# Optimization experiments

Measured on AMD Instinct MI355X. Metric: run time of the kernel, lower is better.

Reference implementation:

```python
import jax, jax.numpy as jnp
import numpy as np

F_DIM = 64
USER_SIZES = [11577, 11, 11, 11, 11, 21, 7]
URL_SIZES = [4733, 21, 7, 11, 11]
USER_OFF = np.concatenate([[0], np.cumsum(USER_SIZES)[:-1]]).astype(np.int64)
URL_OFF = np.concatenate([[0], np.cumsum(URL_SIZES)[:-1]]).astype(np.int64)
EPS = 1e-6


def feature_embed(table, offsets, feats):
    # feats: [..., F] int ids per feature column; sum of per-column embeddings -> [..., F_DIM]
    return jnp.take(table, feats + offsets, axis=0).sum(axis=-2)


def cosine(a, b):
    # cosine similarity along last axis, torch-style eps clamping of each norm
    dot = jnp.sum(a * b, axis=-1)
    na = jnp.maximum(jnp.sqrt(jnp.sum(a * a, axis=-1)), EPS)
    nb = jnp.maximum(jnp.sqrt(jnp.sum(b * b, axis=-1)), EPS)
    return dot / (na * nb)


def graph_attention(f_embed, weight_list, center_embed):
    # f_embed: [..., K, D], weight_list: [..., K], center_embed: [..., D]
    cw = cosine(f_embed, jnp.expand_dims(center_embed, -2))      # [..., K]
    cw = jax.nn.softmax(cw, axis=-1)
    new = jax.nn.relu(f_embed * weight_list[..., None]) * cw[..., None]
    return new.sum(axis=-2)                                      # [..., D]


def linear(x, W, b):
    return x @ W.T + b


def setup_inputs() -> dict:
    key = jax.random.key(0)
    ks = jax.random.split(key, 24)
    N, K = 8192, 8
    ri = lambda k, shp, hi: jax.random.randint(k, shp, 0, hi, dtype=jnp.int64)
    rf = lambda k, shp: jax.random.uniform(k, shp, dtype=jnp.float32)
    rn = lambda k, shp, s: jax.random.normal(k, shp, dtype=jnp.float32) * s
    inp = {
        'url_idxs': ri(ks[0], (N,), 4733),
        'user_f_list': ri(ks[1], (N, 7), 7),
        'url_f_list': ri(ks[2], (N, 5), 7),
        'user_1_user_f_list': ri(ks[3], (N, K, 7), 7),
        'user_1_user_weight': rf(ks[4], (N, K)),
        'user_1_url_f_list': ri(ks[5], (N, K, 5), 7),
        'user_1_url_weight': rf(ks[6], (N, K)),
        'user_2_user_f_list': ri(ks[7], (N, K, K, 7), 7),
        'user_2_user_weight': rf(ks[8], (N, K, K)),
        'user_2_url_f_list': ri(ks[9], (N, K, K, 5), 7),
        'user_2_url_weight': rf(ks[10], (N, K, K)),
        'url_2_user_f_list': ri(ks[11], (N, K, K, 7), 7),
        'url_2_user_weight': rf(ks[12], (N, K, K)),
        'url_2_url_f_list': ri(ks[13], (N, K, K, 5), 7),
        'url_2_url_weight': rf(ks[14], (N, K, K)),
        'user_table': rn(ks[15], (int(sum(USER_SIZES)), F_DIM), 0.1),
        'url_table': rn(ks[16], (int(sum(URL_SIZES)), F_DIM), 0.1),
        'W2': rn(ks[17], (F_DIM, 2 * F_DIM), 0.05), 'b2': jnp.zeros((F_DIM,), jnp.float32),
        'W1': rn(ks[18], (F_DIM, 2 * F_DIM), 0.05), 'b1': jnp.zeros((F_DIM,), jnp.float32),
        'Wo': rn(ks[19], (2, 2 * F_DIM), 0.05), 'bo': jnp.zeros((2,), jnp.float32),
    }
    return inp


def reference(url_idxs, user_f_list, url_f_list,
              user_1_user_f_list, user_1_user_weight,
              user_1_url_f_list, user_1_url_weight,
              user_2_user_f_list, user_2_user_weight,
              user_2_url_f_list, user_2_url_weight,
              url_2_user_f_list, url_2_user_weight,
              url_2_url_f_list, url_2_url_weight,
              user_table, url_table, W2, b2, W1, b1, Wo, bo):
    user_off = jnp.asarray(USER_OFF)
    url_off = jnp.asarray(URL_OFF)

    # --- url branch (hop2 -> hop1) ---
    ori_user_1_url = feature_embed(url_table, url_off, user_1_url_f_list)        # [N,K,D]
    ori_url_2_user = feature_embed(user_table, user_off, url_2_user_f_list)      # [N,K,K,D]
    url_2_user_new = graph_attention(ori_url_2_user, url_2_user_weight, ori_user_1_url)
    ori_url_2_url = feature_embed(url_table, url_off, url_2_url_f_list)
    url_2_url_new = graph_attention(ori_url_2_url, url_2_url_weight, ori_user_1_url)
    user_1_url = (url_2_user_new + url_2_url_new) / 2
    user_1_url = jax.nn.relu(linear(jnp.concatenate([ori_user_1_url, user_1_url], axis=2), W2, b2))

    # --- user branch (hop2 -> hop1) ---
    ori_user_1_user = feature_embed(user_table, user_off, user_1_user_f_list)
    ori_user_2_user = feature_embed(user_table, user_off, user_2_user_f_list)
    user_2_user_new = graph_attention(ori_user_2_user, user_2_user_weight, ori_user_1_user)
    ori_user_2_url = feature_embed(url_table, url_off, user_2_url_f_list)
    user_2_url_new = graph_attention(ori_user_2_url, user_2_url_weight, ori_user_1_user)
    user_1_user = (user_2_user_new + user_2_url_new) / 2
    user_1_user = jax.nn.relu(linear(jnp.concatenate([ori_user_1_user, user_1_user], axis=2), W2, b2))

    # --- hop1 -> center ---
    ori_user = feature_embed(user_table, user_off, user_f_list)                  # [N,D]
    u1_url_new = graph_attention(user_1_url, user_1_url_weight, ori_user)
    u1_user_new = graph_attention(user_1_user, user_1_user_weight, ori_user)
    user_embed = (u1_url_new + u1_user_new) / 2
    user_embed = jax.nn.relu(linear(jnp.concatenate([ori_user, user_embed], axis=1), W1, b1))

    url_embed = feature_embed(url_table, url_off, url_f_list)                    # [N,D]
    out = linear(jnp.concatenate([user_embed, url_embed], axis=1), Wo, bo)       # [N,2]
    return jax.nn.softmax(out, axis=1)
```

## Files before the change

kernel.cpp:

```cpp
#include <hip/hip_runtime.h>

#define TPB 256
#define SPB 4
#define NSAMP 8192

#if __has_builtin(__builtin_amdgcn_rcpf)
#define RCPF(x) __builtin_amdgcn_rcpf(x)
#else
#define RCPF(x) (1.0f/(x))
#endif
#if __has_builtin(__builtin_amdgcn_rsqf)
#define RSQF(x) __builtin_amdgcn_rsqf(x)
#else
#define RSQF(x) rsqrtf(x)
#endif

#define O_CENT   0
#define O_CRN    1024
#define O_ORI    1040
#define O_ORN    1104
#define O_URLEMB 1108
#define O_JOB    1172
#define O_H1     2196
#define O_PIDX   3220
#define O_W      3428
#define O_GA1    3684
#define O_PART   3812
#define O_W1H    4068
#define O_CIDX   4084
#define DYN_SZ   4096

__device__ __forceinline__ float sx(float v, int m) { return __shfl_xor(v, m, 64); }

template <int CTRL>
__device__ __forceinline__ float dpp_add(float v) {
  return v + __int_as_float(__builtin_amdgcn_update_dpp(
      0, __float_as_int(v), CTRL, 0xf, 0xf, true));
}
__device__ __forceinline__ float red16(float v) {
  v = dpp_add<0xB1>(v);
  v = dpp_add<0x4E>(v);
  v = dpp_add<0x141>(v);
  v = dpp_add<0x140>(v);
  return v;
}

__global__ __launch_bounds__(TPB, 3)
void gcn_fused(const int* __restrict__ g_user_f, const int* __restrict__ g_url_f,
               const int* __restrict__ g_u1u_f, const float* __restrict__ g_u1u_w,
               const int* __restrict__ g_u1l_f, const float* __restrict__ g_u1l_w,
               const int* __restrict__ g_u2u_f, const float* __restrict__ g_u2u_w,
               const int* __restrict__ g_u2l_f, const float* __restrict__ g_u2l_w,
               const int* __restrict__ g_l2u_f, const float* __restrict__ g_l2u_w,
               const int* __restrict__ g_l2l_f, const float* __restrict__ g_l2l_w,
               const float* __restrict__ g_utab, const float* __restrict__ g_ltab,
               const float* __restrict__ g_W2, const float* __restrict__ g_b2,
               const float* __restrict__ g_W1, const float* __restrict__ g_b1,
               const float* __restrict__ g_Wo, const float* __restrict__ g_bo,
               float* __restrict__ g_out)
{
  __shared__ __align__(16) float s_lut[5376];
  __shared__ __align__(16) float s_dyn[DYN_SZ];

  const int tid  = threadIdx.x;
  const int wv   = tid >> 6;
  const int lane = tid & 63;
  const int g    = (tid >> 4) & 3;
  const int l    = tid & 15;

  float* s_ulut = s_lut;
  float* s_llut = s_lut + 49*64;
  int*   s_pidx = (int*)&s_dyn[O_PIDX];
  int*   s_cidx = (int*)&s_dyn[O_CIDX];
  float* s_h1   = &s_dyn[O_H1];

  float w2r[32];
  for (int half = 0; half < 2; ++half) {
    for (int i = tid; i < 4096; i += TPB) {
      const int r = i >> 7, j = i & 127;
      s_lut[r*132 + j] = g_W2[(half*32 + r)*128 + j];
    }
    __syncthreads();
    if ((lane >> 5) == half) {
      const int lr = lane & 31;
      #pragma unroll
      for (int jj = 0; jj < 32; ++jj)
        w2r[jj] = s_lut[lr*132 + wv*32 + jj];
    }
    __syncthreads();
  }

  {
    constexpr int uoff[7] = {0,11577,11588,11599,11610,11621,11642};
    #pragma unroll
    for (int c = 0; c < 7; ++c)
      for (int i = tid; i < 448; i += TPB)
        s_ulut[c*448 + i] = g_utab[(uoff[c] + (i >> 6))*64 + (i & 63)];
    constexpr int loff[5] = {0,4733,4754,4761,4772};
    #pragma unroll
    for (int c = 0; c < 5; ++c)
      for (int i = tid; i < 448; i += TPB)
        s_llut[c*448 + i] = g_ltab[(loff[c] + (i >> 6))*64 + (i & 63)];
  }

  const float b2v = g_b2[lane];

  const int  jb      = wv;
  const bool F7      = (jb == 0 || jb == 2);
  const int  F3      = F7 ? 7 : 5;
  const float* lut3  = F7 ? s_ulut : s_llut;
  const int  nibbase = (jb == 0) ? 768 : (jb == 1) ? 1216 : (jb == 2) ? 0 : 448;
  const int  b3      = jb >> 1;

  #pragma unroll 1
  for (int s = 0; s < SPB; ++s) {
    const int n = blockIdx.x * SPB + s;
    __syncthreads();

    if (tid < 192) {
      const int w = tid;
      const int* ptr; int rel;
      if (w < 56)       { ptr = g_u2u_f + n*448; rel = w; }
      else if (w < 96)  { ptr = g_u2l_f + n*320; rel = w - 56; }
      else if (w < 152) { ptr = g_l2u_f + n*448; rel = w - 96; }
      else              { ptr = g_l2l_f + n*320; rel = w - 152; }
      const int4 a = *(const int4*)(ptr + rel*8);
      const int4 b = *(const int4*)(ptr + rel*8 + 4);
      s_pidx[w] = (a.x&7) | ((a.y&7)<<4) | ((a.z&7)<<8) | ((a.w&7)<<12)
                | ((b.x&7)<<16) | ((b.y&7)<<20) | ((b.z&7)<<24) | ((b.w&7)<<28);
    } else if (tid < 204) {
      const int w = tid - 192;
      const int* ptr; int rel;
      if (w < 7) { ptr = g_u1u_f + n*56; rel = w; } else { ptr = g_u1l_f + n*40; rel = w - 7; }
      const int4 a = *(const int4*)(ptr + rel*8);
      const int4 b = *(const int4*)(ptr + rel*8 + 4);
      s_pidx[192 + w] = (a.x&7) | ((a.y&7)<<4) | ((a.z&7)<<8) | ((a.w&7)<<12)
                      | ((b.x&7)<<16) | ((b.y&7)<<20) | ((b.z&7)<<24) | ((b.w&7)<<28);
    } else if (tid < 216) {
      const int t = tid - 204;
      s_cidx[t] = (t < 7) ? g_user_f[n*7 + t] : g_url_f[n*5 + (t - 7)];
    } else if (tid < 232) {
      const int t = tid - 216;
      s_dyn[O_W1H + t] = (t < 8) ? g_u1u_w[n*8 + t] : g_u1l_w[n*8 + (t - 8)];
    }
    if (tid < 64) {
      const float* wp = (tid < 16) ? g_l2u_w : (tid < 32) ? g_l2l_w
                       : (tid < 48) ? g_u2u_w : g_u2l_w;
      *(float4*)&s_dyn[O_W + (tid >> 4)*64 + (tid & 15)*4] =
          *(const float4*)&wp[n*64 + (tid & 15)*4];
    }
    *(float4*)&s_dyn[O_JOB + tid*4] = make_float4(0.f, 0.f, 0.f, 0.f);
    #pragma unroll
    for (int r = 0; r < 4; ++r) s_h1[(wv*4 + r)*64 + lane] = b2v;
    __syncthreads();

    {
      const int gg = tid >> 4;
      const bool isUser = gg >= 8;
      const int k = gg & 7;
      const float* lut = isUser ? s_ulut : s_llut;
      const int nb = isUser ? (1536 + k*7) : (1592 + k*5);
      const int wq = nb >> 3;
      unsigned long long u =
          ((unsigned long long)(unsigned)s_pidx[wq + 1] << 32) | (unsigned)s_pidx[wq];
      u >>= ((nb & 7) << 2);
      float4 e = make_float4(0.f,0.f,0.f,0.f);
      if (isUser) {
        #pragma unroll
        for (int c = 0; c < 7; ++c) {
          const int id = (int)(u >> (c*4)) & 7;
          const float4 t = *(const float4*)&lut[((c*7 + id) << 6) + (l << 2)];
          e.x += t.x; e.y += t.y; e.z += t.z; e.w += t.w;
        }
      } else {
        #pragma unroll
        for (int c = 0; c < 5; ++c) {
          const int id = (int)(u >> (c*4)) & 7;
          const float4 t = *(const float4*)&lut[((c*7 + id) << 6) + (l << 2)];
          e.x += t.x; e.y += t.y; e.z += t.z; e.w += t.w;
        }
      }
      float na2 = e.x*e.x + e.y*e.y + e.z*e.z + e.w*e.w;
      na2 = red16(na2);
      const int bsel = isUser ? 1 : 0;
      *(float4*)&s_dyn[O_CENT + bsel*512 + k*64 + l*4] = e;
      if (l == 0) s_dyn[O_CRN + bsel*8 + k] = RSQF(fmaxf(na2, 1e-12f));

      if (gg < 2) {
        const float* lutm = (gg == 0) ? s_ulut : s_llut;
        const int Fm  = (gg == 0) ? 7 : 5;
        const int ibm = (gg == 0) ? 0 : 7;
        float4 em = make_float4(0.f,0.f,0.f,0.f);
        for (int c = 0; c < Fm; ++c) {
          const int id = s_cidx[ibm + c];
          const float4 t = *(const float4*)&lutm[((c*7 + id) << 6) + (l << 2)];
          em.x += t.x; em.y += t.y; em.z += t.z; em.w += t.w;
        }
        if (gg == 0) {
          float nn = em.x*em.x + em.y*em.y + em.z*em.z + em.w*em.w;
          nn = red16(nn);
          *(float4*)&s_dyn[O_ORI + l*4] = em;
          if (l == 0) s_dyn[O_ORN] = RSQF(fmaxf(nn, 1e-12f));
        } else {
          *(float4*)&s_dyn[O_URLEMB + l*4] = em;
        }
      }
    }
    __syncthreads();

    {
      const float* wb = &s_dyn[O_W + jb*64];
      for (int k1 = 0; k1 < 8; ++k1) {
        const float4 c4 = *(const float4*)&s_dyn[O_CENT + b3*512 + k1*64 + l*4];
        const float rnb = s_dyn[O_CRN + b3*8 + k1];
        float4 ek0, ek1; float cs0, cs1;
        #pragma unroll
        for (int p = 0; p < 2; ++p) {
          const int node = k1*8 + p*4 + g;
          const int nb = nibbase + node*F3;
          const int wq = nb >> 3;
          unsigned long long u =
              ((unsigned long long)(unsigned)s_pidx[wq + 1] << 32) | (unsigned)s_pidx[wq];
          u >>= ((nb & 7) << 2);
          float4 e = make_float4(0.f,0.f,0.f,0.f);
          if (F7) {
            #pragma unroll
            for (int c = 0; c < 7; ++c) {
              const int id = (int)(u >> (c*4)) & 7;
              const float4 t = *(const float4*)&lut3[((c*7 + id) << 6) + (l << 2)];
              e.x += t.x; e.y += t.y; e.z += t.z; e.w += t.w;
            }
          } else {
            #pragma unroll
            for (int c = 0; c < 5; ++c) {
              const int id = (int)(u >> (c*4)) & 7;
              const float4 t = *(const float4*)&lut3[((c*7 + id) << 6) + (l << 2)];
              e.x += t.x; e.y += t.y; e.z += t.z; e.w += t.w;
            }
          }
          float dot = e.x*c4.x + e.y*c4.y + e.z*c4.z + e.w*c4.w;
          float na2 = e.x*e.x + e.y*e.y + e.z*e.z + e.w*e.w;
          dot = red16(dot);
          na2 = red16(na2);
          const float cs = dot * RSQF(fmaxf(na2, 1e-12f)) * rnb;
          if (p == 0) { ek0 = e; cs0 = cs; } else { ek1 = e; cs1 = cs; }
        }
        const float ex0 = __expf(cs0), ex1 = __expf(cs1);
        float ss = ex0 + ex1;
        ss += sx(ss, 16); ss += sx(ss, 32);
        const float w0 = wb[k1*8 + g], w1 = wb[k1*8 + 4 + g];
        float ax = fmaxf(ek0.x*w0, 0.f)*ex0 + fmaxf(ek1.x*w1, 0.f)*ex1;
        float ay = fmaxf(ek0.y*w0, 0.f)*ex0 + fmaxf(ek1.y*w1, 0.f)*ex1;
        float az = fmaxf(ek0.z*w0, 0.f)*ex0 + fmaxf(ek1.z*w1, 0.f)*ex1;
        float aw = fmaxf(ek0.w*w0, 0.f)*ex0 + fmaxf(ek1.w*w1, 0.f)*ex1;
        ax += sx(ax,16); ay += sx(ay,16); az += sx(az,16); aw += sx(aw,16);
        ax += sx(ax,32); ay += sx(ay,32); az += sx(az,32); aw += sx(aw,32);
        if (g == 0) {
          const float sc = 0.5f * RCPF(ss);
          float* jp = &s_dyn[O_JOB + b3*512 + k1*64 + l*4];
          atomicAdd(jp + 0, ax*sc);
          atomicAdd(jp + 1, ay*sc);
          atomicAdd(jp + 2, az*sc);
          atomicAdd(jp + 3, aw*sc);
        }
      }
    }
    __syncthreads();

    for (int rr = 0; rr < 16; ++rr) {
      const int branch = rr >> 3, k = rr & 7;
      const float* xp = (wv < 2)
          ? &s_dyn[O_CENT + branch*512 + k*64 + wv*32]
          : &s_dyn[O_JOB  + branch*512 + k*64 + (wv - 2)*32];
      float a = 0.f;
      #pragma unroll
      for (int j4 = 0; j4 < 8; ++j4) {
        const float4 xv = *(const float4*)&xp[j4*4];
        a += xv.x*w2r[j4*4+0] + xv.y*w2r[j4*4+1] + xv.z*w2r[j4*4+2] + xv.w*w2r[j4*4+3];
      }
      atomicAdd(&s_h1[rr*64 + lane], a);
    }
    __syncthreads();
    {
      float4* hp = (float4*)&s_h1[tid*4];
      float4 v = *hp;
      v.x = fmaxf(v.x, 0.f); v.y = fmaxf(v.y, 0.f);
      v.z = fmaxf(v.z, 0.f); v.w = fmaxf(v.w, 0.f);
      *hp = v;
    }
    __syncthreads();

    if (wv < 2) {
      const float4 c4 = *(const float4*)&s_dyn[O_ORI + l*4];
      const float rno = s_dyn[O_ORN];
      const float* h1b = &s_h1[wv*512];
      const int wofs = (wv == 0) ? 8 : 0;
      float4 ek0, ek1; float cs0, cs1;
      #pragma unroll
      for (int p = 0; p < 2; ++p) {
        const int k = p*4 + g;
        const float4 e = *(const float4*)&h1b[k*64 + l*4];
        float dot = e.x*c4.x + e.y*c4.y + e.z*c4.z + e.w*c4.w;
        float na2 = e.x*e.x + e.y*e.y + e.z*e.z + e.w*e.w;
        dot = red16(dot);
        na2 = red16(na2);
        const float cs = dot * RSQF(fmaxf(na2, 1e-12f)) * rno;
        if (p == 0) { ek0 = e; cs0 = cs; } else { ek1 = e; cs1 = cs; }
      }
      const float ex0 = __expf(cs0), ex1 = __expf(cs1);
      float ss = ex0 + ex1;
      ss += sx(ss, 16); ss += sx(ss, 32);
      const float w0 = s_dyn[O_W1H + wofs + g], w1 = s_dyn[O_W1H + wofs + 4 + g];
      float ax = fmaxf(ek0.x*w0, 0.f)*ex0 + fmaxf(ek1.x*w1, 0.f)*ex1;
      float ay = fmaxf(ek0.y*w0, 0.f)*ex0 + fmaxf(ek1.y*w1, 0.f)*ex1;
      float az = fmaxf(ek0.z*w0, 0.f)*ex0 + fmaxf(ek1.z*w1, 0.f)*ex1;
      float aw = fmaxf(ek0.w*w0, 0.f)*ex0 + fmaxf(ek1.w*w1, 0.f)*ex1;
      ax += sx(ax,16); ay += sx(ay,16); az += sx(az,16); aw += sx(aw,16);
      ax += sx(ax,32); ay += sx(ay,32); az += sx(az,32); aw += sx(az,32)*0.f + sx(aw,32);
      if (g == 0) {
        const float sc = 0.5f * RCPF(ss);
        *(float4*)&s_dyn[O_GA1 + wv*64 + l*4] =
            make_float4(ax*sc, ay*sc, az*sc, aw*sc);
      }
    }
    __syncthreads();

    {
      const float* w1p = g_W1 + lane*128 + wv*32;
      float a = 0.f;
      if (wv < 2) {
        const float* xp = &s_dyn[O_ORI + wv*32];
        #pragma unroll
        for (int j4 = 0; j4 < 8; ++j4) {
          const float4 xv = *(const float4*)&xp[j4*4];
          const float4 wq = *(const float4*)&w1p[j4*4];
          a += xv.x*wq.x + xv.y*wq.y + xv.z*wq.z + xv.w*wq.w;
        }
      } else {
        const float* xa = &s_dyn[O_GA1 + (wv - 2)*32];
        const float* xb = &s_dyn[O_GA1 + 64 + (wv - 2)*32];
        #pragma unroll
        for (int j4 = 0; j4 < 8; ++j4) {
          const float4 va = *(const float4*)&xa[j4*4];
          const float4 vb = *(const float4*)&xb[j4*4];
          const float4 wq = *(const float4*)&w1p[j4*4];
          a += (va.x+vb.x)*wq.x + (va.y+vb.y)*wq.y
             + (va.z+vb.z)*wq.z + (va.w+vb.w)*wq.w;
        }
      }
      s_dyn[O_PART + wv*64 + lane] = a;
    }
    __syncthreads();

    if (wv == 0) {
      float ue = g_b1[lane];
      #pragma unroll
      for (int q = 0; q < 4; ++q) ue += s_dyn[O_PART + q*64 + lane];
      ue = fmaxf(ue, 0.f);
      const float ul = s_dyn[O_URLEMB + lane];
      float p0 = ue*g_Wo[lane]     + ul*g_Wo[64 + lane];
      float p1 = ue*g_Wo[128+lane] + ul*g_Wo[192 + lane];
      p0 = red16(p0); p0 += sx(p0, 16); p0 += sx(p0, 32);
      p1 = red16(p1); p1 += sx(p1, 16); p1 += sx(p1, 32);
      if (lane == 0) {
        const float l0 = p0 + g_bo[0], l1 = p1 + g_bo[1];
        const float mx = fmaxf(l0, l1);
        const float q0 = __expf(l0 - mx), q1 = __expf(l1 - mx);
        const float rinv = RCPF(q0 + q1);
        g_out[n*2 + 0] = q0 * rinv;
        g_out[n*2 + 1] = q1 * rinv;
      }
    }
  }
}

extern "C" void kernel_launch(void* const* d_in, const int* in_sizes, int n_in,
                              void* d_out, int out_size, void* d_ws, size_t ws_size,
                              hipStream_t stream) {
  (void)in_sizes; (void)n_in; (void)d_ws; (void)ws_size; (void)out_size;
  const int*   g_user_f = (const int*)d_in[1];
  const int*   g_url_f  = (const int*)d_in[2];
  const int*   g_u1u_f  = (const int*)d_in[3];
  const float* g_u1u_w  = (const float*)d_in[4];
  const int*   g_u1l_f  = (const int*)d_in[5];
  const float* g_u1l_w  = (const float*)d_in[6];
  const int*   g_u2u_f  = (const int*)d_in[7];
  const float* g_u2u_w  = (const float*)d_in[8];
  const int*   g_u2l_f  = (const int*)d_in[9];
  const float* g_u2l_w  = (const float*)d_in[10];
  const int*   g_l2u_f  = (const int*)d_in[11];
  const float* g_l2u_w  = (const float*)d_in[12];
  const int*   g_l2l_f  = (const int*)d_in[13];
  const float* g_l2l_w  = (const float*)d_in[14];
  const float* g_utab   = (const float*)d_in[15];
  const float* g_ltab   = (const float*)d_in[16];
  const float* g_W2     = (const float*)d_in[17];
  const float* g_b2     = (const float*)d_in[18];
  const float* g_W1     = (const float*)d_in[19];
  const float* g_b1     = (const float*)d_in[20];
  const float* g_Wo     = (const float*)d_in[21];
  const float* g_bo     = (const float*)d_in[22];

  gcn_fused<<<NSAMP / SPB, TPB, 0, stream>>>(
      g_user_f, g_url_f, g_u1u_f, g_u1u_w, g_u1l_f, g_u1l_w,
      g_u2u_f, g_u2u_w, g_u2l_f, g_u2l_w, g_l2u_f, g_l2u_w, g_l2l_f, g_l2l_w,
      g_utab, g_ltab, g_W2, g_b2, g_W1, g_b1, g_Wo, g_bo,
      (float*)d_out);
}
```

Before: 537.8 us.

## Remap hop-2 attention so each lane-group owns whole hop-1 nodes, drop syncs

```diff
diff --git a/kernel.cpp b/kernel.cpp
--- a/kernel.cpp
+++ b/kernel.cpp
@@ -1,7 +1,7 @@
 #include <hip/hip_runtime.h>
 
 #define TPB 256
-#define SPB 4
+#define SPB 8
 #define NSAMP 8192
 
 #if __has_builtin(__builtin_amdgcn_rcpf)
@@ -115,7 +115,6 @@
   #pragma unroll 1
   for (int s = 0; s < SPB; ++s) {
     const int n = blockIdx.x * SPB + s;
-    __syncthreads();
 
     if (tid < 192) {
       const int w = tid;
@@ -209,19 +208,25 @@
     __syncthreads();
 
     {
-      const float* wb = &s_dyn[O_W + jb*64];
-      for (int k1 = 0; k1 < 8; ++k1) {
+      #pragma unroll 1
+      for (int pp = 0; pp < 2; ++pp) {
+        const int k1 = pp*4 + g;
         const float4 c4 = *(const float4*)&s_dyn[O_CENT + b3*512 + k1*64 + l*4];
         const float rnb = s_dyn[O_CRN + b3*8 + k1];
-        float4 ek0, ek1; float cs0, cs1;
-        #pragma unroll
-        for (int p = 0; p < 2; ++p) {
-          const int node = k1*8 + p*4 + g;
-          const int nb = nibbase + node*F3;
+        unsigned long long uu[8];
+        #pragma unroll
+        for (int kk = 0; kk < 8; ++kk) {
+          const int nb = nibbase + (k1*8 + kk)*F3;
           const int wq = nb >> 3;
-          unsigned long long u =
+          const unsigned long long u =
               ((unsigned long long)(unsigned)s_pidx[wq + 1] << 32) | (unsigned)s_pidx[wq];
-          u >>= ((nb & 7) << 2);
+          uu[kk] = u >> ((nb & 7) << 2);
+        }
+        float den = 0.f;
+        float nx = 0.f, ny = 0.f, nz = 0.f, nw = 0.f;
+        #pragma unroll
+        for (int kk = 0; kk < 8; ++kk) {
+          const unsigned long long u = uu[kk];
           float4 e = make_float4(0.f,0.f,0.f,0.f);
           if (F7) {
             #pragma unroll
@@ -243,26 +248,20 @@
           dot = red16(dot);
           na2 = red16(na2);
           const float cs = dot * RSQF(fmaxf(na2, 1e-12f)) * rnb;
-          if (p == 0) { ek0 = e; cs0 = cs; } else { ek1 = e; cs1 = cs; }
-        }
-        const float ex0 = __expf(cs0), ex1 = __expf(cs1);
-        float ss = ex0 + ex1;
-        ss += sx(ss, 16); ss += sx(ss, 32);
-        const float w0 = wb[k1*8 + g], w1 = wb[k1*8 + 4 + g];
-        float ax = fmaxf(ek0.x*w0, 0.f)*ex0 + fmaxf(ek1.x*w1, 0.f)*ex1;
-        float ay = fmaxf(ek0.y*w0, 0.f)*ex0 + fmaxf(ek1.y*w1, 0.f)*ex1;
-        float az = fmaxf(ek0.z*w0, 0.f)*ex0 + fmaxf(ek1.z*w1, 0.f)*ex1;
-        float aw = fmaxf(ek0.w*w0, 0.f)*ex0 + fmaxf(ek1.w*w1, 0.f)*ex1;
-        ax += sx(ax,16); ay += sx(ay,16); az += sx(az,16); aw += sx(aw,16);
-        ax += sx(ax,32); ay += sx(ay,32); az += sx(az,32); aw += sx(aw,32);
-        if (g == 0) {
-          const float sc = 0.5f * RCPF(ss);
-          float* jp = &s_dyn[O_JOB + b3*512 + k1*64 + l*4];
-          atomicAdd(jp + 0, ax*sc);
-          atomicAdd(jp + 1, ay*sc);
-          atomicAdd(jp + 2, az*sc);
-          atomicAdd(jp + 3, aw*sc);
-        }
+          const float ex = __expf(cs);
+          const float wk = s_dyn[O_W + jb*64 + k1*8 + kk];
+          den += ex;
+          nx += fmaxf(e.x*wk, 0.f)*ex;
+          ny += fmaxf(e.y*wk, 0.f)*ex;
+          nz += fmaxf(e.z*wk, 0.f)*ex;
+          nw += fmaxf(e.w*wk, 0.f)*ex;
+        }
+        const float sc = 0.5f * RCPF(den);
+        float* jp = &s_dyn[O_JOB + b3*512 + k1*64 + l*4];
+        atomicAdd(jp + 0, nx*sc);
+        atomicAdd(jp + 1, ny*sc);
+        atomicAdd(jp + 2, nz*sc);
+        atomicAdd(jp + 3, nw*sc);
       }
     }
     __syncthreads();
@@ -281,14 +280,6 @@
       atomicAdd(&s_h1[rr*64 + lane], a);
     }
     __syncthreads();
-    {
-      float4* hp = (float4*)&s_h1[tid*4];
-      float4 v = *hp;
-      v.x = fmaxf(v.x, 0.f); v.y = fmaxf(v.y, 0.f);
-      v.z = fmaxf(v.z, 0.f); v.w = fmaxf(v.w, 0.f);
-      *hp = v;
-    }
-    __syncthreads();
 
     if (wv < 2) {
       const float4 c4 = *(const float4*)&s_dyn[O_ORI + l*4];
@@ -299,7 +290,9 @@
       #pragma unroll
       for (int p = 0; p < 2; ++p) {
         const int k = p*4 + g;
-        const float4 e = *(const float4*)&h1b[k*64 + l*4];
+        const float4 eh = *(const float4*)&h1b[k*64 + l*4];
+        const float4 e = make_float4(fmaxf(eh.x,0.f), fmaxf(eh.y,0.f),
+                                     fmaxf(eh.z,0.f), fmaxf(eh.w,0.f));
         float dot = e.x*c4.x + e.y*c4.y + e.z*c4.z + e.w*c4.w;
         float na2 = e.x*e.x + e.y*e.y + e.z*e.z + e.w*e.w;
         dot = red16(dot);
@@ -316,7 +309,7 @@
       float az = fmaxf(ek0.z*w0, 0.f)*ex0 + fmaxf(ek1.z*w1, 0.f)*ex1;
       float aw = fmaxf(ek0.w*w0, 0.f)*ex0 + fmaxf(ek1.w*w1, 0.f)*ex1;
       ax += sx(ax,16); ay += sx(ay,16); az += sx(az,16); aw += sx(aw,16);
-      ax += sx(ax,32); ay += sx(ay,32); az += sx(az,32); aw += sx(az,32)*0.f + sx(aw,32);
+      ax += sx(ax,32); ay += sx(ay,32); az += sx(az,32); aw += sx(aw,32);
       if (g == 0) {
         const float sc = 0.5f * RCPF(ss);
         *(float4*)&s_dyn[O_GA1 + wv*64 + l*4] =
```

Result: slower. 564.4 us (+4.9%).
